# Kernel tuning notes

Measured on AMD Instinct MI355X. Metric: run time of the kernel, lower is better.

The kernel has to match this reference:

```python
import jax, jax.numpy as jnp
import numpy as np

EMB = 256
HEADS = 8

def setup_inputs() -> dict:
    key = jax.random.key(0)
    ks = jax.random.split(key, 8)
    b, t, e, h = 8, 1024, EMB, HEADS
    x = jax.random.normal(ks[0], (b, t, e), dtype=jnp.float32)
    mask_idx = jax.random.randint(ks[1], (b, t, 1), 0, 2, dtype=jnp.int32)
    s = 1.0 / np.sqrt(e)
    Wq = jax.random.normal(ks[2], (e, e * h), dtype=jnp.float32) * s
    Wk = jax.random.normal(ks[3], (e, e * h), dtype=jnp.float32) * s
    Wv = jax.random.normal(ks[4], (e, e * h), dtype=jnp.float32) * s
    Wu = jax.random.normal(ks[5], (h * e, e), dtype=jnp.float32) * (1.0 / np.sqrt(h * e))
    bu = jnp.zeros((e,), dtype=jnp.float32)
    return {"x": x, "mask_idx": mask_idx, "Wq": Wq, "Wk": Wk, "Wv": Wv, "Wu": Wu, "bu": bu}

def reference(x, mask_idx, Wq, Wk, Wv, Wu, bu):
    b, t, e = x.shape
    h = HEADS
    # project and split heads: (b,t,h,e) -> (b,h,t,e)
    q = (x @ Wq).reshape(b, t, h, e).transpose(0, 2, 1, 3)
    k = (x @ Wk).reshape(b, t, h, e).transpose(0, 2, 1, 3)
    v = (x @ Wv).reshape(b, t, h, e).transpose(0, 2, 1, 3)
    scale = e ** 0.25
    q = q / scale
    k = k / scale
    dot = jnp.einsum('bhte,bhse->bhts', q, k)  # (b,h,t,t)
    m = mask_idx.astype(x.dtype)  # (b,t,1)
    mm = jnp.einsum('bti,bsi->bts', m, m)[:, None]  # (b,1,t,t), outer-product mask
    attn = jax.nn.softmax(dot * mm + (1.0 - mm) * (-1e30), axis=-1)
    out = jnp.einsum('bhts,bhse->bhte', attn, v)  # (b,h,t,e)
    out = out.transpose(0, 2, 1, 3).reshape(b, t, h * e)
    return out @ Wu + bu
```

## Files before the change

kernel.cpp:

```cpp
#include <hip/hip_runtime.h>

#define BB 8
#define TT 1024
#define EE 256
#define HH 8
#define BH 64
#define MM 8192
#define NQKV 2048

typedef __attribute__((ext_vector_type(8))) short bf16x8;
typedef __attribute__((ext_vector_type(4))) float f32x4;

__device__ __forceinline__ unsigned short f2bf(float f) {
  unsigned int u = __float_as_uint(f);
  u += 0x7fff + ((u >> 16) & 1);
  return (unsigned short)(u >> 16);
}

__global__ void k_convert_x(const float4* __restrict__ x, ushort4* __restrict__ xb, int n4) {
  int i = blockIdx.x * 256 + threadIdx.x;
  if (i < n4) {
    float4 f = x[i];
    ushort4 o;
    o.x = f2bf(f.x); o.y = f2bf(f.y); o.z = f2bf(f.z); o.w = f2bf(f.w);
    xb[i] = o;
  }
}

__global__ void k_prep_w(const float* __restrict__ Wq, const float* __restrict__ Wk,
                         const float* __restrict__ Wv, const float* __restrict__ Wu,
                         unsigned short* __restrict__ Wtq, unsigned short* __restrict__ Wtk,
                         unsigned short* __restrict__ Wtv, unsigned short* __restrict__ Wut) {
  __shared__ float tile[32][33];
  int z = blockIdx.y;
  const float* in = (z == 0) ? Wq : (z == 1) ? Wk : (z == 2) ? Wv : Wu;
  unsigned short* out = (z == 0) ? Wtq : (z == 1) ? Wtk : (z == 2) ? Wtv : Wut;
  int K = (z < 3) ? EE : NQKV;
  int N = (z < 3) ? NQKV : EE;
  float scale = (z < 2) ? 0.25f : 1.0f;
  int nb = N / 32;
  int bx = blockIdx.x % nb, by = blockIdx.x / nb;
  int n0 = bx * 32, k0 = by * 32;
  int tx = threadIdx.x & 31, ty = threadIdx.x >> 5;
#pragma unroll
  for (int p = 0; p < 4; p++) tile[ty + 8 * p][tx] = in[(size_t)(k0 + ty + 8 * p) * N + (n0 + tx)];
  __syncthreads();
#pragma unroll
  for (int p = 0; p < 4; p++)
    out[(size_t)(n0 + ty + 8 * p) * K + (k0 + tx)] = f2bf(scale * tile[tx][ty + 8 * p]);
}

__global__ __launch_bounds__(256) void k_gemm_qkv(
    const unsigned short* __restrict__ xb,
    const unsigned short* __restrict__ Wtq,
    const unsigned short* __restrict__ Wtk,
    const unsigned short* __restrict__ Wtv,
    unsigned short* __restrict__ qo,
    unsigned short* __restrict__ ko,
    unsigned short* __restrict__ vto) {
  __shared__ unsigned short sh[2 * 128 * 72];
  unsigned short* As = sh;
  unsigned short* Bs = sh + 128 * 72;
  const unsigned short* Bw = (blockIdx.z == 0) ? Wtq : (blockIdx.z == 1 ? Wtk : Wtv);
  int tid = threadIdx.x, lane = tid & 63, w = tid >> 6;
  int wr = w >> 1, wc = w & 1;
  int m0 = blockIdx.y * 128, n0 = blockIdx.x * 128;
  f32x4 acc[4][4] = {};
  for (int kt = 0; kt < 4; kt++) {
    __syncthreads();
    const unsigned short* ga = xb + (size_t)m0 * 256 + kt * 64;
    const unsigned short* gb = Bw + (size_t)n0 * 256 + kt * 64;
#pragma unroll
    for (int p = 0; p < 4; p++) {
      int c = p * 256 + tid, row = c >> 3, col = (c & 7) * 8;
      *(bf16x8*)&As[row * 72 + col] = *(const bf16x8*)&ga[(size_t)row * 256 + col];
      *(bf16x8*)&Bs[row * 72 + col] = *(const bf16x8*)&gb[(size_t)row * 256 + col];
    }
    __syncthreads();
#pragma unroll
    for (int kk = 0; kk < 2; kk++) {
      bf16x8 af[4], bfr[4];
#pragma unroll
      for (int mi = 0; mi < 4; mi++)
        af[mi] = *(bf16x8*)&As[(wr * 64 + mi * 16 + (lane & 15)) * 72 + kk * 32 + (lane >> 4) * 8];
#pragma unroll
      for (int ni = 0; ni < 4; ni++)
        bfr[ni] = *(bf16x8*)&Bs[(wc * 64 + ni * 16 + (lane & 15)) * 72 + kk * 32 + (lane >> 4) * 8];
#pragma unroll
      for (int mi = 0; mi < 4; mi++)
#pragma unroll
        for (int ni = 0; ni < 4; ni++)
          acc[mi][ni] = __builtin_amdgcn_mfma_f32_16x16x32_bf16(af[mi], bfr[ni], acc[mi][ni], 0, 0, 0);
    }
  }
  __syncthreads();
  unsigned short* ob = sh + w * (64 * 72);
  int gm0 = m0 + wr * 64, gn0 = n0 + wc * 64;
  int bb = gm0 >> 10, t0 = gm0 & 1023, hh = gn0 >> 8, d0 = gn0 & 255;
  if (blockIdx.z != 2) {
#pragma unroll
    for (int mi = 0; mi < 4; mi++)
#pragma unroll
      for (int ni = 0; ni < 4; ni++)
#pragma unroll
        for (int i = 0; i < 4; i++)
          ob[(mi * 16 + (lane >> 4) * 4 + i) * 72 + ni * 16 + (lane & 15)] = f2bf(acc[mi][ni][i]);
    unsigned short* outp = (blockIdx.z == 0) ? qo : ko;
    unsigned short* dst = outp + ((size_t)(bb * HH + hh) * TT + t0) * EE + d0;
#pragma unroll
    for (int p = 0; p < 8; p++) {
      int row = (lane >> 3) + 8 * p, col = (lane & 7) * 8;
      *(bf16x8*)&dst[(size_t)row * EE + col] = *(bf16x8*)&ob[row * 72 + col];
    }
  } else {
#pragma unroll
    for (int mi = 0; mi < 4; mi++)
#pragma unroll
      for (int ni = 0; ni < 4; ni++)
#pragma unroll
        for (int i = 0; i < 4; i++)
          ob[(ni * 16 + (lane & 15)) * 72 + mi * 16 + (lane >> 4) * 4 + i] = f2bf(acc[mi][ni][i]);
    unsigned short* dst = vto + ((size_t)(bb * HH + hh) * EE + d0) * TT + t0;
#pragma unroll
    for (int p = 0; p < 8; p++) {
      int row = (lane >> 3) + 8 * p, col = (lane & 7) * 8;
      *(bf16x8*)&dst[(size_t)row * TT + col] = *(bf16x8*)&ob[row * 72 + col];
    }
  }
}

#define KV 32
#define NT (TT / KV)
__global__ __launch_bounds__(256, 2) void k_flash(
    const unsigned short* __restrict__ q,
    const unsigned short* __restrict__ k,
    const unsigned short* __restrict__ vt,
    const int* __restrict__ mask,
    unsigned short* __restrict__ ao) {
  __shared__ unsigned short Ks[2 * 32 * 264];
  __shared__ unsigned short Vs[2 * 256 * 40];
  __shared__ unsigned short Ps[4 * 16 * 40];
  int tid = threadIdx.x, lane = tid & 63, w = tid >> 6;
  int L = blockIdx.x;
  int wg = (L & 7) * 128 + (L >> 3);
  int qt = wg & 15, bh = wg >> 4;
  int b = bh >> 3, hh = bh & 7;
  const unsigned short* qbase = q + ((size_t)bh * TT + qt * 64) * EE;
  const unsigned short* kbase = k + (size_t)bh * TT * EE;
  const unsigned short* vbase = vt + (size_t)bh * EE * TT;

  bf16x8 kpre[4], vpre[4];
#pragma unroll
  for (int p = 0; p < 4; p++) {
    int c = p * 256 + tid;
    kpre[p] = *(const bf16x8*)&kbase[(size_t)(c >> 5) * EE + (c & 31) * 8];
    vpre[p] = *(const bf16x8*)&vbase[(size_t)(c >> 2) * TT + (c & 3) * 8];
  }
#pragma unroll
  for (int p = 0; p < 8; p++) {
    int c = p * 256 + tid, row = c >> 5, col = (c & 31) * 8;
    *(bf16x8*)&Ks[row * 264 + col] = *(const bf16x8*)&qbase[(size_t)row * EE + col];
  }
  __syncthreads();
  bf16x8 qr[8];
#pragma unroll
  for (int kk = 0; kk < 8; kk++)
    qr[kk] = *(bf16x8*)&Ks[(w * 16 + (lane & 15)) * 264 + kk * 32 + (lane >> 4) * 8];
  __syncthreads();
#pragma unroll
  for (int p = 0; p < 4; p++) {
    int c = p * 256 + tid;
    *(bf16x8*)&Ks[(c >> 5) * 264 + (c & 31) * 8] = kpre[p];
    *(bf16x8*)&Vs[(c >> 2) * 40 + (c & 3) * 8] = vpre[p];
  }
  __syncthreads();

  int mq[4];
#pragma unroll
  for (int i = 0; i < 4; i++)
    mq[i] = mask[b * TT + qt * 64 + w * 16 + (lane >> 4) * 4 + i];

  float mrow[4], lrow[4];
  f32x4 oacc[16] = {};
#pragma unroll
  for (int i = 0; i < 4; i++) { mrow[i] = -1e30f; lrow[i] = 0.0f; }

  int cur = 0;
  for (int kt = 0; kt < NT; kt++) {
    if (kt < NT - 1) {
#pragma unroll
      for (int p = 0; p < 4; p++) {
        int c = p * 256 + tid;
        kpre[p] = *(const bf16x8*)&kbase[(size_t)((kt + 1) * KV + (c >> 5)) * EE + (c & 31) * 8];
        vpre[p] = *(const bf16x8*)&vbase[(size_t)(c >> 2) * TT + (kt + 1) * KV + (c & 3) * 8];
      }
    }
    const unsigned short* Kc = Ks + cur * (32 * 264);
    const unsigned short* Vc = Vs + cur * (256 * 40);

    f32x4 sacc[2] = {};
#pragma unroll
    for (int kk = 0; kk < 8; kk++) {
#pragma unroll
      for (int fc = 0; fc < 2; fc++) {
        bf16x8 bfr = *(const bf16x8*)&Kc[(fc * 16 + (lane & 15)) * 264 + kk * 32 + (lane >> 4) * 8];
        sacc[fc] = __builtin_amdgcn_mfma_f32_16x16x32_bf16(qr[kk], bfr, sacc[fc], 0, 0, 0);
      }
    }

    int msv[2];
#pragma unroll
    for (int fc = 0; fc < 2; fc++) msv[fc] = mask[b * TT + kt * KV + fc * 16 + (lane & 15)];
    float pv[2][4], rmax[4];
#pragma unroll
    for (int i = 0; i < 4; i++) rmax[i] = -1e30f;
#pragma unroll
    for (int fc = 0; fc < 2; fc++)
#pragma unroll
      for (int i = 0; i < 4; i++) {
        float s = (mq[i] && msv[fc]) ? sacc[fc][i] : -1e30f;
        pv[fc][i] = s;
        rmax[i] = fmaxf(rmax[i], s);
      }
#pragma unroll
    for (int off = 1; off < 16; off <<= 1)
#pragma unroll
      for (int i = 0; i < 4; i++) rmax[i] = fmaxf(rmax[i], __shfl_xor(rmax[i], off));
    bool need = false;
#pragma unroll
    for (int i = 0; i < 4; i++) need |= (rmax[i] - mrow[i] > 8.0f);
    if (__any(need)) {
      float sc[4];
#pragma unroll
      for (int i = 0; i < 4; i++) {
        float mn = fmaxf(mrow[i], rmax[i]);
        sc[i] = __expf(mrow[i] - mn);
        mrow[i] = mn;
        lrow[i] *= sc[i];
      }
#pragma unroll
      for (int f = 0; f < 16; f++)
#pragma unroll
        for (int i = 0; i < 4; i++) oacc[f][i] *= sc[i];
    }
    float rsum[4] = {0.f, 0.f, 0.f, 0.f};
#pragma unroll
    for (int fc = 0; fc < 2; fc++)
#pragma unroll
      for (int i = 0; i < 4; i++) {
        float pe = __expf(pv[fc][i] - mrow[i]);
        pv[fc][i] = pe;
        rsum[i] += pe;
      }
#pragma unroll
    for (int off = 1; off < 16; off <<= 1)
#pragma unroll
      for (int i = 0; i < 4; i++) rsum[i] += __shfl_xor(rsum[i], off);
#pragma unroll
    for (int i = 0; i < 4; i++) lrow[i] += rsum[i];

    unsigned short* Pw = Ps + w * (16 * 40);
#pragma unroll
    for (int fc = 0; fc < 2; fc++)
#pragma unroll
      for (int i = 0; i < 4; i++)
        Pw[((lane >> 4) * 4 + i) * 40 + fc * 16 + (lane & 15)] = f2bf(pv[fc][i]);
    bf16x8 pa = *(const bf16x8*)&Pw[(lane & 15) * 40 + (lane >> 4) * 8];
#pragma unroll
    for (int ff = 0; ff < 16; ff++) {
      bf16x8 vb = *(const bf16x8*)&Vc[(ff * 16 + (lane & 15)) * 40 + (lane >> 4) * 8];
      oacc[ff] = __builtin_amdgcn_mfma_f32_16x16x32_bf16(pa, vb, oacc[ff], 0, 0, 0);
    }

    if (kt < NT - 1) {
      unsigned short* Kn = Ks + (cur ^ 1) * (32 * 264);
      unsigned short* Vn = Vs + (cur ^ 1) * (256 * 40);
#pragma unroll
      for (int p = 0; p < 4; p++) {
        int c = p * 256 + tid;
        *(bf16x8*)&Kn[(c >> 5) * 264 + (c & 31) * 8] = kpre[p];
        *(bf16x8*)&Vn[(c >> 2) * 40 + (c & 3) * 8] = vpre[p];
      }
      __syncthreads();
    }
    cur ^= 1;
  }

  float inv[4];
#pragma unroll
  for (int i = 0; i < 4; i++) inv[i] = 1.0f / lrow[i];
#pragma unroll
  for (int f = 0; f < 16; f++)
#pragma unroll
    for (int i = 0; i < 4; i++) oacc[f][i] *= inv[i];
  unsigned short* Pw = Ps + w * (16 * 40);
  int t0 = qt * 64 + w * 16;
#pragma unroll
  for (int c2 = 0; c2 < 8; c2++) {
#pragma unroll
    for (int f2 = 0; f2 < 2; f2++) {
      int f = c2 * 2 + f2;
#pragma unroll
      for (int i = 0; i < 4; i++)
        Pw[((lane >> 4) * 4 + i) * 40 + f2 * 16 + (lane & 15)] = f2bf(oacc[f][i]);
    }
    int row = lane >> 2, colg = (lane & 3) * 8;
    bf16x8 vv = *(const bf16x8*)&Pw[row * 40 + colg];
    *(bf16x8*)&ao[((size_t)(b * TT + t0 + row)) * NQKV + hh * EE + c2 * 32 + colg] = vv;
  }
}

__global__ __launch_bounds__(256) void k_gemm_out(
    const unsigned short* __restrict__ A,
    const unsigned short* __restrict__ Wut,
    const float* __restrict__ bu,
    float* __restrict__ out) {
  __shared__ unsigned short As[128 * 72];
  __shared__ unsigned short Bs[64 * 72];
  int tid = threadIdx.x, lane = tid & 63, w = tid >> 6;
  int wr = w >> 1, wc = w & 1;
  int m0 = blockIdx.y * 128, n0 = blockIdx.x * 64;
  f32x4 acc[4][2] = {};
  for (int kt = 0; kt < 32; kt++) {
    __syncthreads();
    const unsigned short* ga = A + (size_t)m0 * 2048 + kt * 64;
    const unsigned short* gb = Wut + (size_t)n0 * 2048 + kt * 64;
#pragma unroll
    for (int p = 0; p < 4; p++) {
      int c = p * 256 + tid, row = c >> 3, col = (c & 7) * 8;
      *(bf16x8*)&As[row * 72 + col] = *(const bf16x8*)&ga[(size_t)row * 2048 + col];
    }
#pragma unroll
    for (int p = 0; p < 2; p++) {
      int c = p * 256 + tid, row = c >> 3, col = (c & 7) * 8;
      *(bf16x8*)&Bs[row * 72 + col] = *(const bf16x8*)&gb[(size_t)row * 2048 + col];
    }
    __syncthreads();
#pragma unroll
    for (int kk = 0; kk < 2; kk++) {
      bf16x8 af[4], bfr[2];
#pragma unroll
      for (int mi = 0; mi < 4; mi++)
        af[mi] = *(bf16x8*)&As[(wr * 64 + mi * 16 + (lane & 15)) * 72 + kk * 32 + (lane >> 4) * 8];
#pragma unroll
      for (int ni = 0; ni < 2; ni++)
        bfr[ni] = *(bf16x8*)&Bs[(wc * 32 + ni * 16 + (lane & 15)) * 72 + kk * 32 + (lane >> 4) * 8];
#pragma unroll
      for (int mi = 0; mi < 4; mi++)
#pragma unroll
        for (int ni = 0; ni < 2; ni++)
          acc[mi][ni] = __builtin_amdgcn_mfma_f32_16x16x32_bf16(af[mi], bfr[ni], acc[mi][ni], 0, 0, 0);
    }
  }
#pragma unroll
  for (int mi = 0; mi < 4; mi++)
#pragma unroll
    for (int ni = 0; ni < 2; ni++) {
      int gm = m0 + wr * 64 + mi * 16 + (lane >> 4) * 4;
      int gn = n0 + wc * 32 + ni * 16 + (lane & 15);
      float bias = bu[gn];
#pragma unroll
      for (int i = 0; i < 4; i++)
        out[(size_t)(gm + i) * EE + gn] = acc[mi][ni][i] + bias;
    }
}

extern "C" void kernel_launch(void* const* d_in, const int* in_sizes, int n_in,
                              void* d_out, int out_size, void* d_ws, size_t ws_size,
                              hipStream_t stream) {
  const float* x  = (const float*)d_in[0];
  const int* mask = (const int*)d_in[1];
  const float* Wq = (const float*)d_in[2];
  const float* Wk = (const float*)d_in[3];
  const float* Wv = (const float*)d_in[4];
  const float* Wu = (const float*)d_in[5];
  const float* bu = (const float*)d_in[6];
  float* out = (float*)d_out;

  char* ws = (char*)d_ws;
  size_t off = 0;
  auto alloc = [&](size_t bytes) {
    char* p = ws + off;
    off += (bytes + 255) & ~(size_t)255;
    return p;
  };
  unsigned short* xb  = (unsigned short*)alloc((size_t)MM * EE * 2);
  unsigned short* Wtq = (unsigned short*)alloc((size_t)NQKV * EE * 2);
  unsigned short* Wtk = (unsigned short*)alloc((size_t)NQKV * EE * 2);
  unsigned short* Wtv = (unsigned short*)alloc((size_t)NQKV * EE * 2);
  unsigned short* Wut = (unsigned short*)alloc((size_t)EE * NQKV * 2);
  unsigned short* qb  = (unsigned short*)alloc((size_t)BH * TT * EE * 2);
  unsigned short* kb  = (unsigned short*)alloc((size_t)BH * TT * EE * 2);
  unsigned short* vtb = (unsigned short*)alloc((size_t)BH * TT * EE * 2);
  unsigned short* ao  = (unsigned short*)alloc((size_t)MM * NQKV * 2);

  hipLaunchKernelGGL(k_convert_x, dim3((MM * EE / 4 + 255) / 256), dim3(256), 0, stream,
                     (const float4*)x, (ushort4*)xb, MM * EE / 4);
  hipLaunchKernelGGL(k_prep_w, dim3(512, 4), dim3(256), 0, stream,
                     Wq, Wk, Wv, Wu, Wtq, Wtk, Wtv, Wut);

  hipLaunchKernelGGL(k_gemm_qkv, dim3(NQKV / 128, MM / 128, 3), dim3(256), 0, stream,
                     xb, Wtq, Wtk, Wtv, qb, kb, vtb);
  hipLaunchKernelGGL(k_flash, dim3(TT / 64 * BH), dim3(256), 0, stream, qb, kb, vtb, mask, ao);
  hipLaunchKernelGGL(k_gemm_out, dim3(EE / 64, MM / 128), dim3(256), 0, stream, ao, Wut, bu, out);
}
```

Measured before the change: 343.8 us.

## Enlarge flash tile to 128 queries and 64-key blocks, drop double buffering

The flash attention kernel now uses 512-thread blocks covering 128 query rows (8 waves) and processes 64-key tiles instead of 32. Each K/V tile loaded into shared memory is reused by twice as many query rows, and there are half as many loop iterations. The register-prefetch double buffering is removed in favour of synchronous loads followed by barriers. Global-load latency is therefore no longer hidden behind compute, and the launch bound of 4 blocks of 512 threads may force register spilling given the 64-float accumulators.

```diff
diff --git a/kernel.cpp b/kernel.cpp
--- a/kernel.cpp
+++ b/kernel.cpp
@@ -129,93 +129,80 @@
   }
 }
 
-#define KV 32
-#define NT (TT / KV)
-__global__ __launch_bounds__(256, 2) void k_flash(
+__global__ __launch_bounds__(512, 4) void k_flash(
     const unsigned short* __restrict__ q,
     const unsigned short* __restrict__ k,
     const unsigned short* __restrict__ vt,
     const int* __restrict__ mask,
     unsigned short* __restrict__ ao) {
-  __shared__ unsigned short Ks[2 * 32 * 264];
-  __shared__ unsigned short Vs[2 * 256 * 40];
-  __shared__ unsigned short Ps[4 * 16 * 40];
+  __shared__ unsigned short Ks[64 * 264];
+  __shared__ unsigned short Vs[256 * 72];
+  __shared__ unsigned short Ps[8 * 16 * 40];
   int tid = threadIdx.x, lane = tid & 63, w = tid >> 6;
   int L = blockIdx.x;
-  int wg = (L & 7) * 128 + (L >> 3);
-  int qt = wg & 15, bh = wg >> 4;
+  int wg = (L & 7) * 64 + (L >> 3);
+  int qt = wg & 7, bh = wg >> 3;
   int b = bh >> 3, hh = bh & 7;
-  const unsigned short* qbase = q + ((size_t)bh * TT + qt * 64) * EE;
+  const unsigned short* qbase = q + ((size_t)bh * TT + qt * 128) * EE;
   const unsigned short* kbase = k + (size_t)bh * TT * EE;
   const unsigned short* vbase = vt + (size_t)bh * EE * TT;
 
-  bf16x8 kpre[4], vpre[4];
-#pragma unroll
-  for (int p = 0; p < 4; p++) {
-    int c = p * 256 + tid;
-    kpre[p] = *(const bf16x8*)&kbase[(size_t)(c >> 5) * EE + (c & 31) * 8];
-    vpre[p] = *(const bf16x8*)&vbase[(size_t)(c >> 2) * TT + (c & 3) * 8];
-  }
-#pragma unroll
-  for (int p = 0; p < 8; p++) {
-    int c = p * 256 + tid, row = c >> 5, col = (c & 31) * 8;
-    *(bf16x8*)&Ks[row * 264 + col] = *(const bf16x8*)&qbase[(size_t)row * EE + col];
-  }
-  __syncthreads();
   bf16x8 qr[8];
 #pragma unroll
-  for (int kk = 0; kk < 8; kk++)
-    qr[kk] = *(bf16x8*)&Ks[(w * 16 + (lane & 15)) * 264 + kk * 32 + (lane >> 4) * 8];
-  __syncthreads();
-#pragma unroll
-  for (int p = 0; p < 4; p++) {
-    int c = p * 256 + tid;
-    *(bf16x8*)&Ks[(c >> 5) * 264 + (c & 31) * 8] = kpre[p];
-    *(bf16x8*)&Vs[(c >> 2) * 40 + (c & 3) * 8] = vpre[p];
-  }
-  __syncthreads();
+  for (int h = 0; h < 2; h++) {
+#pragma unroll
+    for (int p = 0; p < 4; p++) {
+      int c = p * 512 + tid, row = c >> 5, col = (c & 31) * 8;
+      *(bf16x8*)&Ks[row * 264 + col] = *(const bf16x8*)&qbase[(size_t)(h * 64 + row) * EE + col];
+    }
+    __syncthreads();
+    if ((w >> 2) == h) {
+#pragma unroll
+      for (int kk = 0; kk < 8; kk++)
+        qr[kk] = *(bf16x8*)&Ks[((w & 3) * 16 + (lane & 15)) * 264 + kk * 32 + (lane >> 4) * 8];
+    }
+    __syncthreads();
+  }
 
   int mq[4];
 #pragma unroll
   for (int i = 0; i < 4; i++)
-    mq[i] = mask[b * TT + qt * 64 + w * 16 + (lane >> 4) * 4 + i];
+    mq[i] = mask[b * TT + qt * 128 + w * 16 + (lane >> 4) * 4 + i];
 
   float mrow[4], lrow[4];
   f32x4 oacc[16] = {};
 #pragma unroll
   for (int i = 0; i < 4; i++) { mrow[i] = -1e30f; lrow[i] = 0.0f; }
 
-  int cur = 0;
-  for (int kt = 0; kt < NT; kt++) {
-    if (kt < NT - 1) {
-#pragma unroll
-      for (int p = 0; p < 4; p++) {
-        int c = p * 256 + tid;
-        kpre[p] = *(const bf16x8*)&kbase[(size_t)((kt + 1) * KV + (c >> 5)) * EE + (c & 31) * 8];
-        vpre[p] = *(const bf16x8*)&vbase[(size_t)(c >> 2) * TT + (kt + 1) * KV + (c & 3) * 8];
-      }
-    }
-    const unsigned short* Kc = Ks + cur * (32 * 264);
-    const unsigned short* Vc = Vs + cur * (256 * 40);
-
-    f32x4 sacc[2] = {};
+  for (int kt = 0; kt < 16; kt++) {
+#pragma unroll
+    for (int p = 0; p < 4; p++) {
+      int c = p * 512 + tid;
+      *(bf16x8*)&Ks[(c >> 5) * 264 + (c & 31) * 8] =
+          *(const bf16x8*)&kbase[(size_t)(kt * 64 + (c >> 5)) * EE + (c & 31) * 8];
+      *(bf16x8*)&Vs[(c >> 3) * 72 + (c & 7) * 8] =
+          *(const bf16x8*)&vbase[(size_t)(c >> 3) * TT + kt * 64 + (c & 7) * 8];
+    }
+    __syncthreads();
+
+    f32x4 sacc[4] = {};
 #pragma unroll
     for (int kk = 0; kk < 8; kk++) {
 #pragma unroll
-      for (int fc = 0; fc < 2; fc++) {
-        bf16x8 bfr = *(const bf16x8*)&Kc[(fc * 16 + (lane & 15)) * 264 + kk * 32 + (lane >> 4) * 8];
+      for (int fc = 0; fc < 4; fc++) {
+        bf16x8 bfr = *(bf16x8*)&Ks[(fc * 16 + (lane & 15)) * 264 + kk * 32 + (lane >> 4) * 8];
         sacc[fc] = __builtin_amdgcn_mfma_f32_16x16x32_bf16(qr[kk], bfr, sacc[fc], 0, 0, 0);
       }
     }
 
-    int msv[2];
-#pragma unroll
-    for (int fc = 0; fc < 2; fc++) msv[fc] = mask[b * TT + kt * KV + fc * 16 + (lane & 15)];
-    float pv[2][4], rmax[4];
+    int msv[4];
+#pragma unroll
+    for (int fc = 0; fc < 4; fc++) msv[fc] = mask[b * TT + kt * 64 + fc * 16 + (lane & 15)];
+    float pv[4][4], rmax[4];
 #pragma unroll
     for (int i = 0; i < 4; i++) rmax[i] = -1e30f;
 #pragma unroll
-    for (int fc = 0; fc < 2; fc++)
+    for (int fc = 0; fc < 4; fc++)
 #pragma unroll
       for (int i = 0; i < 4; i++) {
         float s = (mq[i] && msv[fc]) ? sacc[fc][i] : -1e30f;
@@ -245,7 +232,7 @@
     }
     float rsum[4] = {0.f, 0.f, 0.f, 0.f};
 #pragma unroll
-    for (int fc = 0; fc < 2; fc++)
+    for (int fc = 0; fc < 4; fc++)
 #pragma unroll
       for (int i = 0; i < 4; i++) {
         float pe = __expf(pv[fc][i] - mrow[i]);
@@ -261,29 +248,22 @@
 
     unsigned short* Pw = Ps + w * (16 * 40);
 #pragma unroll
-    for (int fc = 0; fc < 2; fc++)
-#pragma unroll
-      for (int i = 0; i < 4; i++)
-        Pw[((lane >> 4) * 4 + i) * 40 + fc * 16 + (lane & 15)] = f2bf(pv[fc][i]);
-    bf16x8 pa = *(const bf16x8*)&Pw[(lane & 15) * 40 + (lane >> 4) * 8];
-#pragma unroll
-    for (int ff = 0; ff < 16; ff++) {
-      bf16x8 vb = *(const bf16x8*)&Vc[(ff * 16 + (lane & 15)) * 40 + (lane >> 4) * 8];
-      oacc[ff] = __builtin_amdgcn_mfma_f32_16x16x32_bf16(pa, vb, oacc[ff], 0, 0, 0);
-    }
-
-    if (kt < NT - 1) {
-      unsigned short* Kn = Ks + (cur ^ 1) * (32 * 264);
-      unsigned short* Vn = Vs + (cur ^ 1) * (256 * 40);
-#pragma unroll
-      for (int p = 0; p < 4; p++) {
-        int c = p * 256 + tid;
-        *(bf16x8*)&Kn[(c >> 5) * 264 + (c & 31) * 8] = kpre[p];
-        *(bf16x8*)&Vn[(c >> 2) * 40 + (c & 3) * 8] = vpre[p];
-      }
-      __syncthreads();
-    }
-    cur ^= 1;
+    for (int kk2 = 0; kk2 < 2; kk2++) {
+#pragma unroll
+      for (int fc2 = 0; fc2 < 2; fc2++) {
+        int fc = kk2 * 2 + fc2;
+#pragma unroll
+        for (int i = 0; i < 4; i++)
+          Pw[((lane >> 4) * 4 + i) * 40 + fc2 * 16 + (lane & 15)] = f2bf(pv[fc][i]);
+      }
+      bf16x8 pa = *(const bf16x8*)&Pw[(lane & 15) * 40 + (lane >> 4) * 8];
+#pragma unroll
+      for (int ff = 0; ff < 16; ff++) {
+        bf16x8 vb = *(bf16x8*)&Vs[(ff * 16 + (lane & 15)) * 72 + kk2 * 32 + (lane >> 4) * 8];
+        oacc[ff] = __builtin_amdgcn_mfma_f32_16x16x32_bf16(pa, vb, oacc[ff], 0, 0, 0);
+      }
+    }
+    __syncthreads();
   }
 
   float inv[4];
@@ -294,7 +274,7 @@
 #pragma unroll
     for (int i = 0; i < 4; i++) oacc[f][i] *= inv[i];
   unsigned short* Pw = Ps + w * (16 * 40);
-  int t0 = qt * 64 + w * 16;
+  int t0 = qt * 128 + w * 16;
 #pragma unroll
   for (int c2 = 0; c2 < 8; c2++) {
 #pragma unroll
@@ -401,6 +381,6 @@
 
   hipLaunchKernelGGL(k_gemm_qkv, dim3(NQKV / 128, MM / 128, 3), dim3(256), 0, stream,
                      xb, Wtq, Wtk, Wtv, qb, kb, vtb);
-  hipLaunchKernelGGL(k_flash, dim3(TT / 64 * BH), dim3(256), 0, stream, qb, kb, vtb, mask, ao);
+  hipLaunchKernelGGL(k_flash, dim3(TT / 128 * BH), dim3(512), 0, stream, qb, kb, vtb, mask, ao);
   hipLaunchKernelGGL(k_gemm_out, dim3(EE / 64, MM / 128), dim3(256), 0, stream, ao, Wut, bu, out);
 }
```

New measurement: 376.7 us. +9.6%, slower.
